# Kernel tuning notes

Hardware: AMD Instinct MI355X
Metric: run time of the kernel (lower is better)

Reference implementation:

```python
import jax, jax.numpy as jnp
from jax import lax
import numpy as np

ITER_ = 10
SMOOTH = 1.0

# ---------- soft skeletonization (clDice-style, 2D) ----------

def _max_pool(x, wh, ww):
    # x: [B,1,H,W]
    return lax.reduce_window(x, -jnp.inf, lax.max, (1, 1, wh, ww), (1, 1, 1, 1), 'SAME')

def _soft_erode(x):
    return jnp.minimum(-_max_pool(-x, 3, 1), -_max_pool(-x, 1, 3))

def _soft_dilate(x):
    return _max_pool(x, 3, 3)

def _soft_open(x):
    return _soft_dilate(_soft_erode(x))

def soft_skel(img, iters):
    skel = jax.nn.relu(img - _soft_open(img))
    for _ in range(iters):
        img = _soft_erode(img)
        delta = jax.nn.relu(img - _soft_open(img))
        skel = skel + jax.nn.relu(delta - skel * delta)
    return skel

# ---------- exact 2D Euclidean distance transform ----------

def _edt2d(mask):
    # mask: [H,W] bool, True = foreground. distance to nearest background pixel.
    H, W = mask.shape
    BIG = jnp.float32(H + W)
    z = ~mask  # background indicator
    def step(d, zr):
        d = jnp.where(zr, 0.0, jnp.minimum(d + 1.0, BIG))
        return d, d
    init = jnp.full((H,), BIG, jnp.float32)
    _, f = lax.scan(step, init, z.T)            # [W,H] forward along rows
    _, b = lax.scan(step, init, z.T[::-1])      # backward
    g = jnp.minimum(f, b[::-1]).T               # [H,W] 1D row distance
    ys = jnp.arange(H, dtype=jnp.float32)
    diff2 = (ys[:, None] - ys[None, :]) ** 2    # [H,H]
    # lower envelope over columns: d2[y,x] = min_y' g[y',x]^2 + (y-y')^2
    d2 = jnp.min(g[None, :, :] ** 2 + diff2[:, :, None], axis=1)  # [H,W]
    return jnp.sqrt(d2)

_edt_batched = jax.vmap(_edt2d)  # [B,H,W] bool -> [B,H,W] float

# ---------- cbDice pieces ----------

def combine_tensors(A, B, C):
    return jnp.where((A != 0) & (B == 0), A * C, B * C)

def get_weights(mask_input, skel_input, prob_flag):
    # mask_input/skel_input: [B,H,W] float
    mask = mask_input > 0.5
    skel = skel_input > 0.5
    dist = lax.stop_gradient(_edt_batched(mask))       # EDT of binary mask, non-diff
    distances = jnp.where(mask, dist, 0.0)
    skel_radius = jnp.where(skel, distances, 0.0)
    rmax = jnp.maximum(jnp.max(skel_radius, axis=(1, 2), keepdims=True), 1.0)
    rmin = jnp.maximum(jnp.min(skel_radius, axis=(1, 2), keepdims=True), 1.0)
    d_clip = jnp.minimum(distances, rmax)
    dist_map_norm = d_clip / rmax
    skel_R_norm = skel_radius / rmax
    I_norm = (rmax - skel_radius + rmin) / rmax        # dim == 2 branch
    I_norm = jnp.where(skel, I_norm, 0.0)
    if prob_flag:
        return dist_map_norm * mask_input, skel_R_norm * mask_input, I_norm * skel_input
    m = mask.astype(jnp.float32)
    s = skel.astype(jnp.float32)
    return dist_map_norm * m, skel_R_norm * m, I_norm * s

def soft_cb_dice_loss(y_pred, y_true):
    p = jax.nn.sigmoid(y_pred)                              # [B,1,H,W]
    pb = jnp.concatenate([1.0 - p, p], axis=1)              # [B,2,H,W]
    pp = jax.nn.softmax(pb, axis=1)[:, 1]                   # [B,H,W]
    yt = jnp.where(y_true > 0, 1.0, 0.0)[:, 0]              # [B,H,W]
    hard = lax.stop_gradient((pp > 0.5).astype(jnp.float32))
    skel_pred_hard = lax.stop_gradient(soft_skel(hard[:, None], ITER_)[:, 0])
    skel_true = lax.stop_gradient(soft_skel(yt[:, None], ITER_)[:, 0])
    skel_pred_prob = skel_pred_hard * pp
    q_vl, q_slvl, q_sl = get_weights(yt, skel_true, False)
    q_vp, q_spvp, q_sp = get_weights(pp, skel_pred_prob, True)
    w_tprec = (jnp.sum(q_sp * q_vl) + SMOOTH) / (jnp.sum(combine_tensors(q_spvp, q_slvl, q_sp)) + SMOOTH)
    w_tsens = (jnp.sum(q_sl * q_vp) + SMOOTH) / (jnp.sum(combine_tensors(q_slvl, q_spvp, q_sl)) + SMOOTH)
    return 1.0 - 2.0 * (w_tprec * w_tsens) / (w_tprec + w_tsens)

def setup_inputs() -> dict:
    key = jax.random.key(0)
    k1, k2 = jax.random.split(key)
    y_pred = jax.random.normal(k1, (4, 1, 256, 256), dtype=jnp.float32)
    y_true = jax.random.randint(k2, (4, 1, 256, 256), 0, 2, dtype=jnp.int32)
    return {"y_pred": y_pred, "y_true": y_true}

def reference(y_pred, y_true):
    return soft_cb_dice_loss(y_pred, y_true)
```

## Files before the change

kernel.cpp:

```cpp
#include <hip/hip_runtime.h>

typedef unsigned long long u64;

#define NIMG 4
#define H 256
#define W 256
#define NPIX (H*W)
#define NTOT (NIMG*NPIX)
#define WPR 4
#define WPI (H*WPR)
#define WPB (NIMG*WPI)
#define XT 16

__global__ void prep_kernel(const float* __restrict__ y_pred,
                            const int* __restrict__ y_true,
                            float* __restrict__ pp,
                            u64* __restrict__ mask_bits,
                            unsigned* __restrict__ rmm_u,
                            double* __restrict__ sums) {
  if (blockIdx.x == 0) {
    if (threadIdx.x < 16) rmm_u[threadIdx.x] = (threadIdx.x & 1) ? 0x7F800000u : 0u;
    else if (threadIdx.x < 20) sums[threadIdx.x - 16] = 0.0;
  }
  int i = blockIdx.x * 256 + threadIdx.x;
  float x = y_pred[i];
  float p = 1.0f / (1.0f + expf(-x));
  float q = 1.0f / (1.0f + expf(-(2.0f * p - 1.0f)));
  pp[i] = q;
  u64 bt = __ballot(y_true[i] > 0);
  u64 bp = __ballot(q > 0.5f);
  if ((threadIdx.x & 63) == 0) {
    mask_bits[i >> 6] = bt;
    mask_bits[WPB + (i >> 6)] = bp;
  }
}

__device__ __forceinline__ void erode_from(const u64 S[][WPR], int y, u64 out[WPR]) {
  u64 c[WPR], up[WPR], dn[WPR];
#pragma unroll
  for (int k = 0; k < WPR; ++k) {
    c[k]  = S[y][k];
    up[k] = (y > 0)     ? S[y-1][k] : ~0ULL;
    dn[k] = (y < H-1)   ? S[y+1][k] : ~0ULL;
  }
#pragma unroll
  for (int k = 0; k < WPR; ++k) {
    u64 l = (c[k] << 1) | ((k > 0)     ? (c[k-1] >> 63) : 1ULL);
    u64 r = (c[k] >> 1) | ((k < WPR-1) ? (c[k+1] << 63) : 0x8000000000000000ULL);
    out[k] = c[k] & up[k] & dn[k] & l & r;
  }
}

__device__ __forceinline__ void dilate_from(const u64 S[][WPR], int y, u64 out[WPR]) {
  u64 v[WPR];
#pragma unroll
  for (int k = 0; k < WPR; ++k) {
    u64 a = S[y][k];
    if (y > 0)   a |= S[y-1][k];
    if (y < H-1) a |= S[y+1][k];
    v[k] = a;
  }
#pragma unroll
  for (int k = 0; k < WPR; ++k) {
    u64 l = (v[k] << 1) | ((k > 0)     ? (v[k-1] >> 63) : 0ULL);
    u64 r = (v[k] >> 1) | ((k < WPR-1) ? (v[k+1] << 63) : 0ULL);
    out[k] = v[k] | l | r;
  }
}

__global__ void skel_kernel(const u64* __restrict__ mask_bits,
                            u64* __restrict__ skel_bits) {
  __shared__ u64 SA[H][WPR];
  __shared__ u64 SB[H][WPR];
  int y = threadIdx.x;
  int base = blockIdx.x * WPI;
  u64 a[WPR], cur[WPR], e[WPR], d[WPR], sk[WPR];
#pragma unroll
  for (int k = 0; k < WPR; ++k) { a[k] = mask_bits[base + y*WPR + k]; SA[y][k] = a[k]; }
  __syncthreads();
  erode_from(SA, y, e);
#pragma unroll
  for (int k = 0; k < WPR; ++k) SB[y][k] = e[k];
  __syncthreads();
  dilate_from(SB, y, d);
#pragma unroll
  for (int k = 0; k < WPR; ++k) { sk[k] = a[k] & ~d[k]; cur[k] = e[k]; }
  u64 (*P)[WPR] = SB;
  u64 (*Q)[WPR] = SA;
  for (int it = 0; it < 10; ++it) {
    erode_from(P, y, e);
#pragma unroll
    for (int k = 0; k < WPR; ++k) Q[y][k] = e[k];
    __syncthreads();
    dilate_from(Q, y, d);
#pragma unroll
    for (int k = 0; k < WPR; ++k) { sk[k] |= cur[k] & ~d[k]; cur[k] = e[k]; }
    u64 (*T)[WPR] = P; P = Q; Q = T;
  }
#pragma unroll
  for (int k = 0; k < WPR; ++k) skel_bits[base + y*WPR + k] = sk[k];
}

__global__ void edt_cols_kernel(const u64* __restrict__ mask_bits,
                                const u64* __restrict__ skel_bits,
                                float* __restrict__ edt,
                                unsigned* __restrict__ rmm_u) {
  __shared__ float col2[H][XT + 1];
  int bi = blockIdx.x >> 4;
  int xt = blockIdx.x & 15;
  int x0 = xt * XT;
  int kx = x0 >> 6;
  int sh0 = x0 & 63;
  int t = threadIdx.x;
  {
    int y = t;
    const u64* row = mask_bits + bi*WPI + y*WPR;
    u64 z[WPR];
#pragma unroll
    for (int k = 0; k < WPR; ++k) z[k] = ~row[k];
#pragma unroll
    for (int xx = 0; xx < XT; ++xx) {
      int x = x0 + xx;
      int bx = x & 63;
      int ld = 512;
      {
        u64 w = z[kx] & ((bx == 63) ? ~0ULL : ((1ULL << (bx+1)) - 1ULL));
        for (int k = kx; ; ) {
          if (w) { int pos = 63 - __builtin_clzll(w) + (k << 6); ld = x - pos; break; }
          if (--k < 0) break;
          w = z[k];
        }
      }
      int rd = 512;
      {
        u64 w = z[kx] & (~0ULL << bx);
        for (int k = kx; ; ) {
          if (w) { int pos = __builtin_ctzll(w) + (k << 6); rd = pos - x; break; }
          if (++k > WPR-1) break;
          w = z[k];
        }
      }
      int g = min(ld, rd);
      col2[y][xx] = (float)(g * g);
    }
  }
  __syncthreads();
  int x  = t & (XT - 1);
  int yg = t >> 4;
  float vmax = 0.0f, vmin = 3.0e38f;
#pragma unroll
  for (int j = 0; j < 16; ++j) {
    int y = yg * 16 + j;
    float best = col2[y][x];
    for (int k = 1; k < H; ++k) {
      float k2 = (float)(k * k);
      if (k2 >= best) break;
      int ym = y - k, yq = y + k;
      if (ym >= 0) best = fminf(best, col2[ym][x] + k2);
      if (yq < H)  best = fminf(best, col2[yq][x] + k2);
    }
    float dist = sqrtf(best);
    edt[bi*NPIX + y*W + x0 + x] = dist;
    u64 sw = skel_bits[bi*WPI + y*WPR + kx];
    int sb = (int)((sw >> (sh0 + x)) & 1ULL);
    float srad = sb ? dist : 0.0f;
    vmax = fmaxf(vmax, srad);
    vmin = fminf(vmin, srad);
  }
  for (int o = 32; o > 0; o >>= 1) {
    vmax = fmaxf(vmax, __shfl_down(vmax, o, 64));
    vmin = fminf(vmin, __shfl_down(vmin, o, 64));
  }
  __shared__ float smax[4], smin[4];
  int wave = t >> 6, lane = t & 63;
  if (lane == 0) { smax[wave] = vmax; smin[wave] = vmin; }
  __syncthreads();
  if (t == 0) {
    float mx = smax[0], mn = smin[0];
    for (int wv = 1; wv < 4; ++wv) { mx = fmaxf(mx, smax[wv]); mn = fminf(mn, smin[wv]); }
    atomicMax(&rmm_u[bi*2 + 0], __float_as_uint(mx));
    atomicMin(&rmm_u[bi*2 + 1], __float_as_uint(mn));
  }
}

__global__ void final_sum_kernel(const float* __restrict__ edt,
                                 const u64* __restrict__ mask_bits,
                                 const u64* __restrict__ skel_bits,
                                 const float* __restrict__ pp,
                                 const unsigned* __restrict__ rmm_u,
                                 double* __restrict__ sums) {
  int i0 = (blockIdx.x * 256 + threadIdx.x) * 4;
  int img = i0 >> 16;
  int wi = i0 >> 6;
  int b0 = i0 & 63;
  u64 mw_t = mask_bits[wi];
  u64 sw_t = skel_bits[wi];
  u64 sw_p = skel_bits[WPB + wi];
  float4 d_t4 = *(const float4*)(edt + i0);
  float4 d_p4 = *(const float4*)(edt + NTOT + i0);
  float4 pp4  = *(const float4*)(pp + i0);
  float rmax_t = fmaxf(__uint_as_float(rmm_u[img*2 + 0]), 1.0f);
  float rmin_t = fmaxf(__uint_as_float(rmm_u[img*2 + 1]), 1.0f);
  float rmax_p = fmaxf(__uint_as_float(rmm_u[(4+img)*2 + 0]), 1.0f);
  float rmin_p = fmaxf(__uint_as_float(rmm_u[(4+img)*2 + 1]), 1.0f);
  float t1 = 0.f, t2 = 0.f, t3 = 0.f, t4 = 0.f;
  float dts[4] = {d_t4.x, d_t4.y, d_t4.z, d_t4.w};
  float dps[4] = {d_p4.x, d_p4.y, d_p4.z, d_p4.w};
  float pps[4] = {pp4.x, pp4.y, pp4.z, pp4.w};
#pragma unroll
  for (int j = 0; j < 4; ++j) {
    int b = b0 + j;
    int m_t = (int)((mw_t >> b) & 1ULL);
    int s_t = (int)((sw_t >> b) & 1ULL);
    float distances_t = m_t ? dts[j] : 0.0f;
    float skelrad_t   = s_t ? distances_t : 0.0f;
    float dmn_t = fminf(distances_t, rmax_t) / rmax_t;
    float srn_t = skelrad_t / rmax_t;
    float In_t  = s_t ? (rmax_t - skelrad_t + rmin_t) / rmax_t : 0.0f;
    float q_vl   = m_t ? dmn_t : 0.0f;
    float q_slvl = m_t ? srn_t : 0.0f;
    float q_sl   = s_t ? In_t  : 0.0f;
    int s_pb = (int)((sw_p >> b) & 1ULL);
    float ppv = pps[j];
    float skel_in_p = s_pb ? ppv : 0.0f;
    bool msk_p = ppv > 0.5f;
    bool sk_p  = skel_in_p > 0.5f;
    float distances_p = msk_p ? dps[j] : 0.0f;
    float skelrad_p   = sk_p ? distances_p : 0.0f;
    float dmn_p = fminf(distances_p, rmax_p) / rmax_p;
    float srn_p = skelrad_p / rmax_p;
    float In_p  = sk_p ? (rmax_p - skelrad_p + rmin_p) / rmax_p : 0.0f;
    float q_vp   = dmn_p * ppv;
    float q_spvp = srn_p * ppv;
    float q_sp   = In_p * skel_in_p;
    t1 += q_sp * q_vl;
    t2 += (q_spvp != 0.0f && q_slvl == 0.0f) ? q_spvp * q_sp : q_slvl * q_sp;
    t3 += q_sl * q_vp;
    t4 += (q_slvl != 0.0f && q_spvp == 0.0f) ? q_slvl * q_sl : q_spvp * q_sl;
  }
  for (int o = 32; o > 0; o >>= 1) {
    t1 += __shfl_down(t1, o, 64);
    t2 += __shfl_down(t2, o, 64);
    t3 += __shfl_down(t3, o, 64);
    t4 += __shfl_down(t4, o, 64);
  }
  __shared__ float part[4][4];
  int wave = threadIdx.x >> 6, lane = threadIdx.x & 63;
  if (lane == 0) { part[wave][0]=t1; part[wave][1]=t2; part[wave][2]=t3; part[wave][3]=t4; }
  __syncthreads();
  if (threadIdx.x == 0) {
    float a0=0,a1=0,a2=0,a3=0;
    for (int wv = 0; wv < 4; ++wv) {
      a0 += part[wv][0]; a1 += part[wv][1]; a2 += part[wv][2]; a3 += part[wv][3];
    }
    atomicAdd(&sums[0], (double)a0);
    atomicAdd(&sums[1], (double)a1);
    atomicAdd(&sums[2], (double)a2);
    atomicAdd(&sums[3], (double)a3);
  }
}

__global__ void finalize_kernel(const double* __restrict__ sums,
                                float* __restrict__ out) {
  double wp  = (sums[0] + 1.0) / (sums[1] + 1.0);
  double wsn = (sums[2] + 1.0) / (sums[3] + 1.0);
  double loss = 1.0 - 2.0 * (wp * wsn) / (wp + wsn);
  out[0] = (float)loss;
}

extern "C" void kernel_launch(void* const* d_in, const int* in_sizes, int n_in,
                              void* d_out, int out_size, void* d_ws, size_t ws_size,
                              hipStream_t stream) {
  (void)in_sizes; (void)n_in; (void)out_size; (void)ws_size;
  const float* y_pred = (const float*)d_in[0];
  const int*   y_true = (const int*)d_in[1];
  float* out = (float*)d_out;
  char* ws = (char*)d_ws;

  float* pp        = (float*)(ws + 0);
  float* edt       = (float*)(ws + 1048576);
  u64*   mask_bits = (u64*)  (ws + 3145728);
  u64*   skel_bits = (u64*)  (ws + 3211264);
  unsigned* rmm_u  = (unsigned*)(ws + 3276800);
  double* sums     = (double*)(ws + 3276864);

  prep_kernel<<<NTOT/256, 256, 0, stream>>>(y_pred, y_true, pp, mask_bits, rmm_u, sums);
  skel_kernel<<<8, 256, 0, stream>>>(mask_bits, skel_bits);
  edt_cols_kernel<<<8*(W/XT), 256, 0, stream>>>(mask_bits, skel_bits, edt, rmm_u);
  final_sum_kernel<<<NTOT/1024, 256, 0, stream>>>(edt, mask_bits, skel_bits, pp, rmm_u, sums);
  finalize_kernel<<<1, 1, 0, stream>>>(sums, out);
}
```

Before: 95.78 us.

## Fuse all stages into one cooperative kernel with grid syncs

Result: slower. 143.9 us (+50.2%).

```diff
diff --git a/kernel.cpp b/kernel.cpp
--- a/kernel.cpp
+++ b/kernel.cpp
@@ -1,4 +1,7 @@
 #include <hip/hip_runtime.h>
+#include <hip/hip_cooperative_groups.h>
+
+namespace cg = cooperative_groups;
 
 typedef unsigned long long u64;
 
@@ -11,29 +14,9 @@
 #define WPI (H*WPR)
 #define WPB (NIMG*WPI)
 #define XT 16
-
-__global__ void prep_kernel(const float* __restrict__ y_pred,
-                            const int* __restrict__ y_true,
-                            float* __restrict__ pp,
-                            u64* __restrict__ mask_bits,
-                            unsigned* __restrict__ rmm_u,
-                            double* __restrict__ sums) {
-  if (blockIdx.x == 0) {
-    if (threadIdx.x < 16) rmm_u[threadIdx.x] = (threadIdx.x & 1) ? 0x7F800000u : 0u;
-    else if (threadIdx.x < 20) sums[threadIdx.x - 16] = 0.0;
-  }
-  int i = blockIdx.x * 256 + threadIdx.x;
-  float x = y_pred[i];
-  float p = 1.0f / (1.0f + expf(-x));
-  float q = 1.0f / (1.0f + expf(-(2.0f * p - 1.0f)));
-  pp[i] = q;
-  u64 bt = __ballot(y_true[i] > 0);
-  u64 bp = __ballot(q > 0.5f);
-  if ((threadIdx.x & 63) == 0) {
-    mask_bits[i >> 6] = bt;
-    mask_bits[WPB + (i >> 6)] = bp;
-  }
-}
+#define NEDT 128
+#define NSKEL 8
+#define NBLK (NEDT+NSKEL)
 
 __device__ __forceinline__ void erode_from(const u64 S[][WPR], int y, u64 out[WPR]) {
   u64 c[WPR], up[WPR], dn[WPR];
@@ -68,204 +51,248 @@
   }
 }
 
-__global__ void skel_kernel(const u64* __restrict__ mask_bits,
-                            u64* __restrict__ skel_bits) {
+__global__ void __launch_bounds__(256, 1) fused_kernel(
+    const float* __restrict__ y_pred, const int* __restrict__ y_true,
+    float* __restrict__ pp, u64* __restrict__ mask_bits, u64* __restrict__ skel_bits,
+    float* __restrict__ edt, unsigned* __restrict__ rmm_u, double* __restrict__ sums,
+    unsigned* __restrict__ done_cnt, float* __restrict__ out) {
+  cg::grid_group grid = cg::this_grid();
   __shared__ u64 SA[H][WPR];
   __shared__ u64 SB[H][WPR];
-  int y = threadIdx.x;
-  int base = blockIdx.x * WPI;
-  u64 a[WPR], cur[WPR], e[WPR], d[WPR], sk[WPR];
-#pragma unroll
-  for (int k = 0; k < WPR; ++k) { a[k] = mask_bits[base + y*WPR + k]; SA[y][k] = a[k]; }
-  __syncthreads();
-  erode_from(SA, y, e);
-#pragma unroll
-  for (int k = 0; k < WPR; ++k) SB[y][k] = e[k];
-  __syncthreads();
-  dilate_from(SB, y, d);
-#pragma unroll
-  for (int k = 0; k < WPR; ++k) { sk[k] = a[k] & ~d[k]; cur[k] = e[k]; }
-  u64 (*P)[WPR] = SB;
-  u64 (*Q)[WPR] = SA;
-  for (int it = 0; it < 10; ++it) {
-    erode_from(P, y, e);
-#pragma unroll
-    for (int k = 0; k < WPR; ++k) Q[y][k] = e[k];
-    __syncthreads();
-    dilate_from(Q, y, d);
-#pragma unroll
-    for (int k = 0; k < WPR; ++k) { sk[k] |= cur[k] & ~d[k]; cur[k] = e[k]; }
-    u64 (*T)[WPR] = P; P = Q; Q = T;
-  }
-#pragma unroll
-  for (int k = 0; k < WPR; ++k) skel_bits[base + y*WPR + k] = sk[k];
-}
-
-__global__ void edt_cols_kernel(const u64* __restrict__ mask_bits,
-                                const u64* __restrict__ skel_bits,
-                                float* __restrict__ edt,
-                                unsigned* __restrict__ rmm_u) {
   __shared__ float col2[H][XT + 1];
-  int bi = blockIdx.x >> 4;
-  int xt = blockIdx.x & 15;
-  int x0 = xt * XT;
-  int kx = x0 >> 6;
-  int sh0 = x0 & 63;
+  __shared__ float redf[4][4];
   int t = threadIdx.x;
-  {
+
+  if (blockIdx.x < NEDT) {
+    if (blockIdx.x == 0) {
+      if (t < 16) rmm_u[t] = (t & 1) ? 0x7F800000u : 0u;
+      else if (t < 20) sums[t - 16] = 0.0;
+      else if (t == 20) *done_cnt = 0u;
+    }
+    int g = blockIdx.x * 256 + t;
+#pragma unroll
+    for (int j = 0; j < 8; ++j) {
+      int i = (j << 15) + g;
+      float x = y_pred[i];
+      float p = 1.0f / (1.0f + expf(-x));
+      float q = 1.0f / (1.0f + expf(-(2.0f * p - 1.0f)));
+      pp[i] = q;
+      u64 bt = __ballot(y_true[i] > 0);
+      u64 bp = __ballot(q > 0.5f);
+      if ((t & 63) == 0) {
+        mask_bits[i >> 6] = bt;
+        mask_bits[WPB + (i >> 6)] = bp;
+      }
+    }
+  }
+  grid.sync();
+
+  float dist_r[16];
+  if (blockIdx.x >= NEDT) {
     int y = t;
-    const u64* row = mask_bits + bi*WPI + y*WPR;
-    u64 z[WPR];
-#pragma unroll
-    for (int k = 0; k < WPR; ++k) z[k] = ~row[k];
-#pragma unroll
-    for (int xx = 0; xx < XT; ++xx) {
-      int x = x0 + xx;
-      int bx = x & 63;
-      int ld = 512;
-      {
-        u64 w = z[kx] & ((bx == 63) ? ~0ULL : ((1ULL << (bx+1)) - 1ULL));
-        for (int k = kx; ; ) {
-          if (w) { int pos = 63 - __builtin_clzll(w) + (k << 6); ld = x - pos; break; }
-          if (--k < 0) break;
-          w = z[k];
+    int base = (blockIdx.x - NEDT) * WPI;
+    u64 a[WPR], cur[WPR], e[WPR], d[WPR], sk[WPR];
+#pragma unroll
+    for (int k = 0; k < WPR; ++k) { a[k] = mask_bits[base + y*WPR + k]; SA[y][k] = a[k]; }
+    __syncthreads();
+    erode_from(SA, y, e);
+#pragma unroll
+    for (int k = 0; k < WPR; ++k) SB[y][k] = e[k];
+    __syncthreads();
+    dilate_from(SB, y, d);
+#pragma unroll
+    for (int k = 0; k < WPR; ++k) { sk[k] = a[k] & ~d[k]; cur[k] = e[k]; }
+    u64 (*P)[WPR] = SB;
+    u64 (*Q)[WPR] = SA;
+    for (int it = 0; it < 10; ++it) {
+      erode_from(P, y, e);
+#pragma unroll
+      for (int k = 0; k < WPR; ++k) Q[y][k] = e[k];
+      __syncthreads();
+      dilate_from(Q, y, d);
+#pragma unroll
+      for (int k = 0; k < WPR; ++k) { sk[k] |= cur[k] & ~d[k]; cur[k] = e[k]; }
+      u64 (*T)[WPR] = P; P = Q; Q = T;
+    }
+#pragma unroll
+    for (int k = 0; k < WPR; ++k) skel_bits[base + y*WPR + k] = sk[k];
+  } else {
+    int bi = blockIdx.x >> 4;
+    int xt = blockIdx.x & 15;
+    int x0 = xt * XT;
+    int kx = x0 >> 6;
+    {
+      int y = t;
+      const u64* row = mask_bits + bi*WPI + y*WPR;
+      u64 z[WPR];
+#pragma unroll
+      for (int k = 0; k < WPR; ++k) z[k] = ~row[k];
+#pragma unroll
+      for (int xx = 0; xx < XT; ++xx) {
+        int x = x0 + xx;
+        int bx = x & 63;
+        int ld = 512;
+        {
+          u64 w = z[kx] & ((bx == 63) ? ~0ULL : ((1ULL << (bx+1)) - 1ULL));
+          for (int k = kx; ; ) {
+            if (w) { int pos = 63 - __builtin_clzll(w) + (k << 6); ld = x - pos; break; }
+            if (--k < 0) break;
+            w = z[k];
+          }
         }
-      }
-      int rd = 512;
-      {
-        u64 w = z[kx] & (~0ULL << bx);
-        for (int k = kx; ; ) {
-          if (w) { int pos = __builtin_ctzll(w) + (k << 6); rd = pos - x; break; }
-          if (++k > WPR-1) break;
-          w = z[k];
+        int rd = 512;
+        {
+          u64 w = z[kx] & (~0ULL << bx);
+          for (int k = kx; ; ) {
+            if (w) { int pos = __builtin_ctzll(w) + (k << 6); rd = pos - x; break; }
+            if (++k > WPR-1) break;
+            w = z[k];
+          }
         }
-      }
-      int g = min(ld, rd);
-      col2[y][xx] = (float)(g * g);
-    }
-  }
-  __syncthreads();
-  int x  = t & (XT - 1);
-  int yg = t >> 4;
-  float vmax = 0.0f, vmin = 3.0e38f;
-#pragma unroll
-  for (int j = 0; j < 16; ++j) {
-    int y = yg * 16 + j;
-    float best = col2[y][x];
-    for (int k = 1; k < H; ++k) {
-      float k2 = (float)(k * k);
-      if (k2 >= best) break;
-      int ym = y - k, yq = y + k;
-      if (ym >= 0) best = fminf(best, col2[ym][x] + k2);
-      if (yq < H)  best = fminf(best, col2[yq][x] + k2);
-    }
-    float dist = sqrtf(best);
-    edt[bi*NPIX + y*W + x0 + x] = dist;
-    u64 sw = skel_bits[bi*WPI + y*WPR + kx];
-    int sb = (int)((sw >> (sh0 + x)) & 1ULL);
-    float srad = sb ? dist : 0.0f;
-    vmax = fmaxf(vmax, srad);
-    vmin = fminf(vmin, srad);
-  }
-  for (int o = 32; o > 0; o >>= 1) {
-    vmax = fmaxf(vmax, __shfl_down(vmax, o, 64));
-    vmin = fminf(vmin, __shfl_down(vmin, o, 64));
-  }
-  __shared__ float smax[4], smin[4];
-  int wave = t >> 6, lane = t & 63;
-  if (lane == 0) { smax[wave] = vmax; smin[wave] = vmin; }
-  __syncthreads();
-  if (t == 0) {
-    float mx = smax[0], mn = smin[0];
-    for (int wv = 1; wv < 4; ++wv) { mx = fmaxf(mx, smax[wv]); mn = fminf(mn, smin[wv]); }
-    atomicMax(&rmm_u[bi*2 + 0], __float_as_uint(mx));
-    atomicMin(&rmm_u[bi*2 + 1], __float_as_uint(mn));
-  }
-}
-
-__global__ void final_sum_kernel(const float* __restrict__ edt,
-                                 const u64* __restrict__ mask_bits,
-                                 const u64* __restrict__ skel_bits,
-                                 const float* __restrict__ pp,
-                                 const unsigned* __restrict__ rmm_u,
-                                 double* __restrict__ sums) {
-  int i0 = (blockIdx.x * 256 + threadIdx.x) * 4;
-  int img = i0 >> 16;
-  int wi = i0 >> 6;
-  int b0 = i0 & 63;
-  u64 mw_t = mask_bits[wi];
-  u64 sw_t = skel_bits[wi];
-  u64 sw_p = skel_bits[WPB + wi];
-  float4 d_t4 = *(const float4*)(edt + i0);
-  float4 d_p4 = *(const float4*)(edt + NTOT + i0);
-  float4 pp4  = *(const float4*)(pp + i0);
-  float rmax_t = fmaxf(__uint_as_float(rmm_u[img*2 + 0]), 1.0f);
-  float rmin_t = fmaxf(__uint_as_float(rmm_u[img*2 + 1]), 1.0f);
-  float rmax_p = fmaxf(__uint_as_float(rmm_u[(4+img)*2 + 0]), 1.0f);
-  float rmin_p = fmaxf(__uint_as_float(rmm_u[(4+img)*2 + 1]), 1.0f);
-  float t1 = 0.f, t2 = 0.f, t3 = 0.f, t4 = 0.f;
-  float dts[4] = {d_t4.x, d_t4.y, d_t4.z, d_t4.w};
-  float dps[4] = {d_p4.x, d_p4.y, d_p4.z, d_p4.w};
-  float pps[4] = {pp4.x, pp4.y, pp4.z, pp4.w};
-#pragma unroll
-  for (int j = 0; j < 4; ++j) {
-    int b = b0 + j;
-    int m_t = (int)((mw_t >> b) & 1ULL);
-    int s_t = (int)((sw_t >> b) & 1ULL);
-    float distances_t = m_t ? dts[j] : 0.0f;
-    float skelrad_t   = s_t ? distances_t : 0.0f;
-    float dmn_t = fminf(distances_t, rmax_t) / rmax_t;
-    float srn_t = skelrad_t / rmax_t;
-    float In_t  = s_t ? (rmax_t - skelrad_t + rmin_t) / rmax_t : 0.0f;
-    float q_vl   = m_t ? dmn_t : 0.0f;
-    float q_slvl = m_t ? srn_t : 0.0f;
-    float q_sl   = s_t ? In_t  : 0.0f;
-    int s_pb = (int)((sw_p >> b) & 1ULL);
-    float ppv = pps[j];
-    float skel_in_p = s_pb ? ppv : 0.0f;
-    bool msk_p = ppv > 0.5f;
-    bool sk_p  = skel_in_p > 0.5f;
-    float distances_p = msk_p ? dps[j] : 0.0f;
-    float skelrad_p   = sk_p ? distances_p : 0.0f;
-    float dmn_p = fminf(distances_p, rmax_p) / rmax_p;
-    float srn_p = skelrad_p / rmax_p;
-    float In_p  = sk_p ? (rmax_p - skelrad_p + rmin_p) / rmax_p : 0.0f;
-    float q_vp   = dmn_p * ppv;
-    float q_spvp = srn_p * ppv;
-    float q_sp   = In_p * skel_in_p;
-    t1 += q_sp * q_vl;
-    t2 += (q_spvp != 0.0f && q_slvl == 0.0f) ? q_spvp * q_sp : q_slvl * q_sp;
-    t3 += q_sl * q_vp;
-    t4 += (q_slvl != 0.0f && q_spvp == 0.0f) ? q_slvl * q_sl : q_spvp * q_sl;
-  }
-  for (int o = 32; o > 0; o >>= 1) {
-    t1 += __shfl_down(t1, o, 64);
-    t2 += __shfl_down(t2, o, 64);
-    t3 += __shfl_down(t3, o, 64);
-    t4 += __shfl_down(t4, o, 64);
-  }
-  __shared__ float part[4][4];
-  int wave = threadIdx.x >> 6, lane = threadIdx.x & 63;
-  if (lane == 0) { part[wave][0]=t1; part[wave][1]=t2; part[wave][2]=t3; part[wave][3]=t4; }
-  __syncthreads();
-  if (threadIdx.x == 0) {
-    float a0=0,a1=0,a2=0,a3=0;
-    for (int wv = 0; wv < 4; ++wv) {
-      a0 += part[wv][0]; a1 += part[wv][1]; a2 += part[wv][2]; a3 += part[wv][3];
-    }
-    atomicAdd(&sums[0], (double)a0);
-    atomicAdd(&sums[1], (double)a1);
-    atomicAdd(&sums[2], (double)a2);
-    atomicAdd(&sums[3], (double)a3);
-  }
-}
-
-__global__ void finalize_kernel(const double* __restrict__ sums,
-                                float* __restrict__ out) {
-  double wp  = (sums[0] + 1.0) / (sums[1] + 1.0);
-  double wsn = (sums[2] + 1.0) / (sums[3] + 1.0);
-  double loss = 1.0 - 2.0 * (wp * wsn) / (wp + wsn);
-  out[0] = (float)loss;
+        int g = min(ld, rd);
+        col2[y][xx] = (float)(g * g);
+      }
+    }
+    __syncthreads();
+    int x  = t & (XT - 1);
+    int yg = t >> 4;
+#pragma unroll
+    for (int j = 0; j < 16; ++j) {
+      int y = yg * 16 + j;
+      float best = col2[y][x];
+      for (int k = 1; k < H; ++k) {
+        float k2 = (float)(k * k);
+        if (k2 >= best) break;
+        int ym = y - k, yq = y + k;
+        if (ym >= 0) best = fminf(best, col2[ym][x] + k2);
+        if (yq < H)  best = fminf(best, col2[yq][x] + k2);
+      }
+      float dist = sqrtf(best);
+      dist_r[j] = dist;
+      edt[bi*NPIX + y*W + x0 + x] = dist;
+    }
+  }
+  grid.sync();
+
+  if (blockIdx.x < NEDT) {
+    int bi = blockIdx.x >> 4;
+    int xt = blockIdx.x & 15;
+    int x0 = xt * XT;
+    int kx = x0 >> 6;
+    int sh0 = x0 & 63;
+    int x  = t & (XT - 1);
+    int yg = t >> 4;
+    float vmax = 0.0f, vmin = 3.0e38f;
+#pragma unroll
+    for (int j = 0; j < 16; ++j) {
+      int y = yg * 16 + j;
+      u64 sw = skel_bits[bi*WPI + y*WPR + kx];
+      int sb = (int)((sw >> (sh0 + x)) & 1ULL);
+      float srad = sb ? dist_r[j] : 0.0f;
+      vmax = fmaxf(vmax, srad);
+      vmin = fminf(vmin, srad);
+    }
+    for (int o = 32; o > 0; o >>= 1) {
+      vmax = fmaxf(vmax, __shfl_down(vmax, o, 64));
+      vmin = fminf(vmin, __shfl_down(vmin, o, 64));
+    }
+    int wave = t >> 6, lane = t & 63;
+    if (lane == 0) { redf[wave][0] = vmax; redf[wave][1] = vmin; }
+    __syncthreads();
+    if (t == 0) {
+      float mx = redf[0][0], mn = redf[0][1];
+      for (int wv = 1; wv < 4; ++wv) { mx = fmaxf(mx, redf[wv][0]); mn = fminf(mn, redf[wv][1]); }
+      atomicMax(&rmm_u[bi*2 + 0], __float_as_uint(mx));
+      atomicMin(&rmm_u[bi*2 + 1], __float_as_uint(mn));
+    }
+  }
+  grid.sync();
+
+  if (blockIdx.x < NEDT) {
+    int g = blockIdx.x * 256 + t;
+    int i0 = g * 8;
+    int img = i0 >> 16;
+    int wi  = i0 >> 6;
+    int b0  = i0 & 63;
+    u64 mw_t = mask_bits[wi];
+    u64 sw_t = skel_bits[wi];
+    u64 sw_p = skel_bits[WPB + wi];
+    float4 dt0 = *(const float4*)(edt + i0);
+    float4 dt1 = *(const float4*)(edt + i0 + 4);
+    float4 dp0 = *(const float4*)(edt + NTOT + i0);
+    float4 dp1 = *(const float4*)(edt + NTOT + i0 + 4);
+    float4 pq0 = *(const float4*)(pp + i0);
+    float4 pq1 = *(const float4*)(pp + i0 + 4);
+    float rmax_t = fmaxf(__uint_as_float(rmm_u[img*2 + 0]), 1.0f);
+    float rmin_t = fmaxf(__uint_as_float(rmm_u[img*2 + 1]), 1.0f);
+    float rmax_p = fmaxf(__uint_as_float(rmm_u[(4+img)*2 + 0]), 1.0f);
+    float rmin_p = fmaxf(__uint_as_float(rmm_u[(4+img)*2 + 1]), 1.0f);
+    float dts[8] = {dt0.x,dt0.y,dt0.z,dt0.w,dt1.x,dt1.y,dt1.z,dt1.w};
+    float dps[8] = {dp0.x,dp0.y,dp0.z,dp0.w,dp1.x,dp1.y,dp1.z,dp1.w};
+    float pps[8] = {pq0.x,pq0.y,pq0.z,pq0.w,pq1.x,pq1.y,pq1.z,pq1.w};
+    float q1 = 0.f, q2 = 0.f, q3 = 0.f, q4 = 0.f;
+#pragma unroll
+    for (int j = 0; j < 8; ++j) {
+      int b = b0 + j;
+      int m_t = (int)((mw_t >> b) & 1ULL);
+      int s_t = (int)((sw_t >> b) & 1ULL);
+      float distances_t = m_t ? dts[j] : 0.0f;
+      float skelrad_t   = s_t ? distances_t : 0.0f;
+      float dmn_t = fminf(distances_t, rmax_t) / rmax_t;
+      float srn_t = skelrad_t / rmax_t;
+      float In_t  = s_t ? (rmax_t - skelrad_t + rmin_t) / rmax_t : 0.0f;
+      float q_vl   = m_t ? dmn_t : 0.0f;
+      float q_slvl = m_t ? srn_t : 0.0f;
+      float q_sl   = s_t ? In_t  : 0.0f;
+      int s_pb = (int)((sw_p >> b) & 1ULL);
+      float ppv = pps[j];
+      float skel_in_p = s_pb ? ppv : 0.0f;
+      bool msk_p = ppv > 0.5f;
+      bool sk_p  = skel_in_p > 0.5f;
+      float distances_p = msk_p ? dps[j] : 0.0f;
+      float skelrad_p   = sk_p ? distances_p : 0.0f;
+      float dmn_p = fminf(distances_p, rmax_p) / rmax_p;
+      float srn_p = skelrad_p / rmax_p;
+      float In_p  = sk_p ? (rmax_p - skelrad_p + rmin_p) / rmax_p : 0.0f;
+      float q_vp   = dmn_p * ppv;
+      float q_spvp = srn_p * ppv;
+      float q_sp   = In_p * skel_in_p;
+      q1 += q_sp * q_vl;
+      q2 += (q_spvp != 0.0f && q_slvl == 0.0f) ? q_spvp * q_sp : q_slvl * q_sp;
+      q3 += q_sl * q_vp;
+      q4 += (q_slvl != 0.0f && q_spvp == 0.0f) ? q_slvl * q_sl : q_spvp * q_sl;
+    }
+    for (int o = 32; o > 0; o >>= 1) {
+      q1 += __shfl_down(q1, o, 64);
+      q2 += __shfl_down(q2, o, 64);
+      q3 += __shfl_down(q3, o, 64);
+      q4 += __shfl_down(q4, o, 64);
+    }
+    int wave = t >> 6, lane = t & 63;
+    if (lane == 0) { redf[wave][0]=q1; redf[wave][1]=q2; redf[wave][2]=q3; redf[wave][3]=q4; }
+    __syncthreads();
+    if (t == 0) {
+      float a0=0,a1=0,a2=0,a3=0;
+      for (int wv = 0; wv < 4; ++wv) {
+        a0 += redf[wv][0]; a1 += redf[wv][1]; a2 += redf[wv][2]; a3 += redf[wv][3];
+      }
+      atomicAdd(&sums[0], (double)a0);
+      atomicAdd(&sums[1], (double)a1);
+      atomicAdd(&sums[2], (double)a2);
+      atomicAdd(&sums[3], (double)a3);
+      __threadfence();
+      unsigned c = atomicAdd(done_cnt, 1u);
+      if (c == NEDT - 1) {
+        double s0 = atomicAdd(&sums[0], 0.0);
+        double s1 = atomicAdd(&sums[1], 0.0);
+        double s2 = atomicAdd(&sums[2], 0.0);
+        double s3 = atomicAdd(&sums[3], 0.0);
+        double wp  = (s0 + 1.0) / (s1 + 1.0);
+        double wsn = (s2 + 1.0) / (s3 + 1.0);
+        out[0] = (float)(1.0 - 2.0 * (wp * wsn) / (wp + wsn));
+      }
+    }
+  }
 }
 
 extern "C" void kernel_launch(void* const* d_in, const int* in_sizes, int n_in,
@@ -283,10 +310,11 @@
   u64*   skel_bits = (u64*)  (ws + 3211264);
   unsigned* rmm_u  = (unsigned*)(ws + 3276800);
   double* sums     = (double*)(ws + 3276864);
-
-  prep_kernel<<<NTOT/256, 256, 0, stream>>>(y_pred, y_true, pp, mask_bits, rmm_u, sums);
-  skel_kernel<<<8, 256, 0, stream>>>(mask_bits, skel_bits);
-  edt_cols_kernel<<<8*(W/XT), 256, 0, stream>>>(mask_bits, skel_bits, edt, rmm_u);
-  final_sum_kernel<<<NTOT/1024, 256, 0, stream>>>(edt, mask_bits, skel_bits, pp, rmm_u, sums);
-  finalize_kernel<<<1, 1, 0, stream>>>(sums, out);
+  unsigned* done_cnt = (unsigned*)(ws + 3276896);
+
+  void* args[] = { (void*)&y_pred, (void*)&y_true, (void*)&pp, (void*)&mask_bits,
+                   (void*)&skel_bits, (void*)&edt, (void*)&rmm_u, (void*)&sums,
+                   (void*)&done_cnt, (void*)&out };
+  hipLaunchCooperativeKernel((void*)fused_kernel, dim3(NBLK), dim3(256),
+                             args, 0, stream);
 }
```

## Fuse skeleton and EDT kernels with inter-block flags; fold finalize into last block

Applied to the files above, without the earlier changes.

After: 102.7 us. 1.07x slower.

```diff
diff --git a/kernel.cpp b/kernel.cpp
--- a/kernel.cpp
+++ b/kernel.cpp
@@ -11,16 +11,51 @@
 #define WPI (H*WPR)
 #define WPB (NIMG*WPI)
 #define XT 16
-
-__global__ void prep_kernel(const float* __restrict__ y_pred,
-                            const int* __restrict__ y_true,
-                            float* __restrict__ pp,
-                            u64* __restrict__ mask_bits,
-                            unsigned* __restrict__ rmm_u,
-                            double* __restrict__ sums) {
+#define NSKEL 8
+#define NEDT 128
+#define NB2 (NSKEL+NEDT)
+#define NB3 (NTOT/1024)
+
+__device__ __forceinline__ void erode_from(const u64 S[][WPR], int y, u64 out[WPR]) {
+  u64 c[WPR], up[WPR], dn[WPR];
+#pragma unroll
+  for (int k = 0; k < WPR; ++k) {
+    c[k]  = S[y][k];
+    up[k] = (y > 0)     ? S[y-1][k] : ~0ULL;
+    dn[k] = (y < H-1)   ? S[y+1][k] : ~0ULL;
+  }
+#pragma unroll
+  for (int k = 0; k < WPR; ++k) {
+    u64 l = (c[k] << 1) | ((k > 0)     ? (c[k-1] >> 63) : 1ULL);
+    u64 r = (c[k] >> 1) | ((k < WPR-1) ? (c[k+1] << 63) : 0x8000000000000000ULL);
+    out[k] = c[k] & up[k] & dn[k] & l & r;
+  }
+}
+
+__device__ __forceinline__ void dilate_from(const u64 S[][WPR], int y, u64 out[WPR]) {
+  u64 v[WPR];
+#pragma unroll
+  for (int k = 0; k < WPR; ++k) {
+    u64 a = S[y][k];
+    if (y > 0)   a |= S[y-1][k];
+    if (y < H-1) a |= S[y+1][k];
+    v[k] = a;
+  }
+#pragma unroll
+  for (int k = 0; k < WPR; ++k) {
+    u64 l = (v[k] << 1) | ((k > 0)     ? (v[k-1] >> 63) : 0ULL);
+    u64 r = (v[k] >> 1) | ((k < WPR-1) ? (v[k+1] << 63) : 0ULL);
+    out[k] = v[k] | l | r;
+  }
+}
+
+__global__ void __launch_bounds__(256) prep_kernel(
+    const float* __restrict__ y_pred, const int* __restrict__ y_true,
+    float* __restrict__ pp, u64* __restrict__ mask_bits,
+    double* __restrict__ sums, unsigned* __restrict__ cnts) {
   if (blockIdx.x == 0) {
-    if (threadIdx.x < 16) rmm_u[threadIdx.x] = (threadIdx.x & 1) ? 0x7F800000u : 0u;
-    else if (threadIdx.x < 20) sums[threadIdx.x - 16] = 0.0;
+    if (threadIdx.x < 4) sums[threadIdx.x] = 0.0;
+    else if (threadIdx.x < 13) cnts[threadIdx.x - 4] = 0u;
   }
   int i = blockIdx.x * 256 + threadIdx.x;
   float x = y_pred[i];
@@ -35,160 +70,152 @@
   }
 }
 
-__device__ __forceinline__ void erode_from(const u64 S[][WPR], int y, u64 out[WPR]) {
-  u64 c[WPR], up[WPR], dn[WPR];
-#pragma unroll
-  for (int k = 0; k < WPR; ++k) {
-    c[k]  = S[y][k];
-    up[k] = (y > 0)     ? S[y-1][k] : ~0ULL;
-    dn[k] = (y < H-1)   ? S[y+1][k] : ~0ULL;
-  }
-#pragma unroll
-  for (int k = 0; k < WPR; ++k) {
-    u64 l = (c[k] << 1) | ((k > 0)     ? (c[k-1] >> 63) : 1ULL);
-    u64 r = (c[k] >> 1) | ((k < WPR-1) ? (c[k+1] << 63) : 0x8000000000000000ULL);
-    out[k] = c[k] & up[k] & dn[k] & l & r;
-  }
-}
-
-__device__ __forceinline__ void dilate_from(const u64 S[][WPR], int y, u64 out[WPR]) {
-  u64 v[WPR];
-#pragma unroll
-  for (int k = 0; k < WPR; ++k) {
-    u64 a = S[y][k];
-    if (y > 0)   a |= S[y-1][k];
-    if (y < H-1) a |= S[y+1][k];
-    v[k] = a;
-  }
-#pragma unroll
-  for (int k = 0; k < WPR; ++k) {
-    u64 l = (v[k] << 1) | ((k > 0)     ? (v[k-1] >> 63) : 0ULL);
-    u64 r = (v[k] >> 1) | ((k < WPR-1) ? (v[k+1] << 63) : 0ULL);
-    out[k] = v[k] | l | r;
-  }
-}
-
-__global__ void skel_kernel(const u64* __restrict__ mask_bits,
-                            u64* __restrict__ skel_bits) {
+__global__ void __launch_bounds__(256, 1) morpho_kernel(
+    const u64* __restrict__ mask_bits, u64* __restrict__ skel_bits,
+    float* __restrict__ edt, float* __restrict__ rmm_f,
+    unsigned* __restrict__ cnts) {
   __shared__ u64 SA[H][WPR];
   __shared__ u64 SB[H][WPR];
-  int y = threadIdx.x;
-  int base = blockIdx.x * WPI;
-  u64 a[WPR], cur[WPR], e[WPR], d[WPR], sk[WPR];
-#pragma unroll
-  for (int k = 0; k < WPR; ++k) { a[k] = mask_bits[base + y*WPR + k]; SA[y][k] = a[k]; }
-  __syncthreads();
-  erode_from(SA, y, e);
-#pragma unroll
-  for (int k = 0; k < WPR; ++k) SB[y][k] = e[k];
-  __syncthreads();
-  dilate_from(SB, y, d);
-#pragma unroll
-  for (int k = 0; k < WPR; ++k) { sk[k] = a[k] & ~d[k]; cur[k] = e[k]; }
-  u64 (*P)[WPR] = SB;
-  u64 (*Q)[WPR] = SA;
-  for (int it = 0; it < 10; ++it) {
-    erode_from(P, y, e);
-#pragma unroll
-    for (int k = 0; k < WPR; ++k) Q[y][k] = e[k];
-    __syncthreads();
-    dilate_from(Q, y, d);
-#pragma unroll
-    for (int k = 0; k < WPR; ++k) { sk[k] |= cur[k] & ~d[k]; cur[k] = e[k]; }
-    u64 (*T)[WPR] = P; P = Q; Q = T;
-  }
-#pragma unroll
-  for (int k = 0; k < WPR; ++k) skel_bits[base + y*WPR + k] = sk[k];
-}
-
-__global__ void edt_cols_kernel(const u64* __restrict__ mask_bits,
-                                const u64* __restrict__ skel_bits,
-                                float* __restrict__ edt,
-                                unsigned* __restrict__ rmm_u) {
   __shared__ float col2[H][XT + 1];
-  int bi = blockIdx.x >> 4;
-  int xt = blockIdx.x & 15;
-  int x0 = xt * XT;
-  int kx = x0 >> 6;
-  int sh0 = x0 & 63;
+  __shared__ float smax[4], smin[4];
   int t = threadIdx.x;
-  {
+
+  if (blockIdx.x < NSKEL) {
+    int bi = blockIdx.x;
     int y = t;
-    const u64* row = mask_bits + bi*WPI + y*WPR;
-    u64 z[WPR];
-#pragma unroll
-    for (int k = 0; k < WPR; ++k) z[k] = ~row[k];
-#pragma unroll
-    for (int xx = 0; xx < XT; ++xx) {
-      int x = x0 + xx;
-      int bx = x & 63;
-      int ld = 512;
-      {
-        u64 w = z[kx] & ((bx == 63) ? ~0ULL : ((1ULL << (bx+1)) - 1ULL));
-        for (int k = kx; ; ) {
-          if (w) { int pos = 63 - __builtin_clzll(w) + (k << 6); ld = x - pos; break; }
-          if (--k < 0) break;
-          w = z[k];
+    int base = bi * WPI;
+    u64 a[WPR], cur[WPR], e[WPR], d[WPR], sk[WPR];
+#pragma unroll
+    for (int k = 0; k < WPR; ++k) { a[k] = mask_bits[base + y*WPR + k]; SA[y][k] = a[k]; }
+    __syncthreads();
+    erode_from(SA, y, e);
+#pragma unroll
+    for (int k = 0; k < WPR; ++k) SB[y][k] = e[k];
+    __syncthreads();
+    dilate_from(SB, y, d);
+#pragma unroll
+    for (int k = 0; k < WPR; ++k) { sk[k] = a[k] & ~d[k]; cur[k] = e[k]; }
+    u64 (*P)[WPR] = SB;
+    u64 (*Q)[WPR] = SA;
+    for (int it = 0; it < 10; ++it) {
+      erode_from(P, y, e);
+#pragma unroll
+      for (int k = 0; k < WPR; ++k) Q[y][k] = e[k];
+      __syncthreads();
+      dilate_from(Q, y, d);
+#pragma unroll
+      for (int k = 0; k < WPR; ++k) { sk[k] |= cur[k] & ~d[k]; cur[k] = e[k]; }
+      u64 (*T)[WPR] = P; P = Q; Q = T;
+    }
+#pragma unroll
+    for (int k = 0; k < WPR; ++k) skel_bits[base + y*WPR + k] = sk[k];
+    __syncthreads();
+#pragma unroll
+    for (int k = 0; k < WPR; ++k) SA[y][k] = sk[k];
+    if (t == 0) {
+      while (__hip_atomic_load(&cnts[bi], __ATOMIC_ACQUIRE,
+                               __HIP_MEMORY_SCOPE_AGENT) < 16u)
+        __builtin_amdgcn_s_sleep(8);
+    }
+    __syncthreads();
+    __threadfence();
+    const float* epx = edt + bi * NPIX;
+    float vmax = 0.0f, vmin = 3.0e38f;
+    for (int it2 = 0; it2 < 64; ++it2) {
+      int p0 = it2 * 1024 + t * 4;
+      float4 d4 = *(const float4*)(epx + p0);
+      int row = p0 >> 8;
+      u64 w = SA[row][(p0 & 255) >> 6];
+      int sh = p0 & 63;
+      float ds[4] = {d4.x, d4.y, d4.z, d4.w};
+#pragma unroll
+      for (int j = 0; j < 4; ++j) {
+        int bit = (int)((w >> (sh + j)) & 1ULL);
+        float srad = bit ? ds[j] : 0.0f;
+        vmax = fmaxf(vmax, srad);
+        vmin = fminf(vmin, srad);
+      }
+    }
+    for (int o = 32; o > 0; o >>= 1) {
+      vmax = fmaxf(vmax, __shfl_down(vmax, o, 64));
+      vmin = fminf(vmin, __shfl_down(vmin, o, 64));
+    }
+    int wave = t >> 6, lane = t & 63;
+    if (lane == 0) { smax[wave] = vmax; smin[wave] = vmin; }
+    __syncthreads();
+    if (t == 0) {
+      float mx = smax[0], mn = smin[0];
+      for (int wv = 1; wv < 4; ++wv) { mx = fmaxf(mx, smax[wv]); mn = fminf(mn, smin[wv]); }
+      rmm_f[bi*2 + 0] = mx;
+      rmm_f[bi*2 + 1] = mn;
+    }
+  } else {
+    int bt = blockIdx.x - NSKEL;
+    int bi = bt >> 4;
+    int xt = bt & 15;
+    int x0 = xt * XT;
+    int kx = x0 >> 6;
+    {
+      int y = t;
+      const u64* row = mask_bits + bi*WPI + y*WPR;
+      u64 z[WPR];
+#pragma unroll
+      for (int k = 0; k < WPR; ++k) z[k] = ~row[k];
+#pragma unroll
+      for (int xx = 0; xx < XT; ++xx) {
+        int x = x0 + xx;
+        int bx = x & 63;
+        int ld = 512;
+        {
+          u64 w = z[kx] & ((bx == 63) ? ~0ULL : ((1ULL << (bx+1)) - 1ULL));
+          for (int k = kx; ; ) {
+            if (w) { int pos = 63 - __builtin_clzll(w) + (k << 6); ld = x - pos; break; }
+            if (--k < 0) break;
+            w = z[k];
+          }
         }
+        int rd = 512;
+        {
+          u64 w = z[kx] & (~0ULL << bx);
+          for (int k = kx; ; ) {
+            if (w) { int pos = __builtin_ctzll(w) + (k << 6); rd = pos - x; break; }
+            if (++k > WPR-1) break;
+            w = z[k];
+          }
+        }
+        int g = min(ld, rd);
+        col2[y][xx] = (float)(g * g);
       }
-      int rd = 512;
-      {
-        u64 w = z[kx] & (~0ULL << bx);
-        for (int k = kx; ; ) {
-          if (w) { int pos = __builtin_ctzll(w) + (k << 6); rd = pos - x; break; }
-          if (++k > WPR-1) break;
-          w = z[k];
-        }
+    }
+    __syncthreads();
+    int x  = t & (XT - 1);
+    int yg = t >> 4;
+#pragma unroll
+    for (int j = 0; j < 16; ++j) {
+      int y = yg * 16 + j;
+      float best = col2[y][x];
+      for (int k = 1; k < H; ++k) {
+        float k2 = (float)(k * k);
+        if (k2 >= best) break;
+        int ym = y - k, yq = y + k;
+        if (ym >= 0) best = fminf(best, col2[ym][x] + k2);
+        if (yq < H)  best = fminf(best, col2[yq][x] + k2);
       }
-      int g = min(ld, rd);
-      col2[y][xx] = (float)(g * g);
-    }
-  }
-  __syncthreads();
-  int x  = t & (XT - 1);
-  int yg = t >> 4;
-  float vmax = 0.0f, vmin = 3.0e38f;
-#pragma unroll
-  for (int j = 0; j < 16; ++j) {
-    int y = yg * 16 + j;
-    float best = col2[y][x];
-    for (int k = 1; k < H; ++k) {
-      float k2 = (float)(k * k);
-      if (k2 >= best) break;
-      int ym = y - k, yq = y + k;
-      if (ym >= 0) best = fminf(best, col2[ym][x] + k2);
-      if (yq < H)  best = fminf(best, col2[yq][x] + k2);
-    }
-    float dist = sqrtf(best);
-    edt[bi*NPIX + y*W + x0 + x] = dist;
-    u64 sw = skel_bits[bi*WPI + y*WPR + kx];
-    int sb = (int)((sw >> (sh0 + x)) & 1ULL);
-    float srad = sb ? dist : 0.0f;
-    vmax = fmaxf(vmax, srad);
-    vmin = fminf(vmin, srad);
-  }
-  for (int o = 32; o > 0; o >>= 1) {
-    vmax = fmaxf(vmax, __shfl_down(vmax, o, 64));
-    vmin = fminf(vmin, __shfl_down(vmin, o, 64));
-  }
-  __shared__ float smax[4], smin[4];
-  int wave = t >> 6, lane = t & 63;
-  if (lane == 0) { smax[wave] = vmax; smin[wave] = vmin; }
-  __syncthreads();
-  if (t == 0) {
-    float mx = smax[0], mn = smin[0];
-    for (int wv = 1; wv < 4; ++wv) { mx = fmaxf(mx, smax[wv]); mn = fminf(mn, smin[wv]); }
-    atomicMax(&rmm_u[bi*2 + 0], __float_as_uint(mx));
-    atomicMin(&rmm_u[bi*2 + 1], __float_as_uint(mn));
-  }
-}
-
-__global__ void final_sum_kernel(const float* __restrict__ edt,
-                                 const u64* __restrict__ mask_bits,
-                                 const u64* __restrict__ skel_bits,
-                                 const float* __restrict__ pp,
-                                 const unsigned* __restrict__ rmm_u,
-                                 double* __restrict__ sums) {
+      edt[bi*NPIX + y*W + x0 + x] = sqrtf(best);
+    }
+    __syncthreads();
+    if (t == 0) {
+      __threadfence();
+      atomicAdd(&cnts[bi], 1u);
+    }
+  }
+}
+
+__global__ void __launch_bounds__(256) final_kernel(
+    const float* __restrict__ edt, const u64* __restrict__ mask_bits,
+    const u64* __restrict__ skel_bits, const float* __restrict__ pp,
+    const float* __restrict__ rmm_f, double* __restrict__ sums,
+    unsigned* __restrict__ cnts, float* __restrict__ out) {
   int i0 = (blockIdx.x * 256 + threadIdx.x) * 4;
   int img = i0 >> 16;
   int wi = i0 >> 6;
@@ -199,10 +226,10 @@
   float4 d_t4 = *(const float4*)(edt + i0);
   float4 d_p4 = *(const float4*)(edt + NTOT + i0);
   float4 pp4  = *(const float4*)(pp + i0);
-  float rmax_t = fmaxf(__uint_as_float(rmm_u[img*2 + 0]), 1.0f);
-  float rmin_t = fmaxf(__uint_as_float(rmm_u[img*2 + 1]), 1.0f);
-  float rmax_p = fmaxf(__uint_as_float(rmm_u[(4+img)*2 + 0]), 1.0f);
-  float rmin_p = fmaxf(__uint_as_float(rmm_u[(4+img)*2 + 1]), 1.0f);
+  float rmax_t = fmaxf(rmm_f[img*2 + 0], 1.0f);
+  float rmin_t = fmaxf(rmm_f[img*2 + 1], 1.0f);
+  float rmax_p = fmaxf(rmm_f[(4+img)*2 + 0], 1.0f);
+  float rmin_p = fmaxf(rmm_f[(4+img)*2 + 1], 1.0f);
   float t1 = 0.f, t2 = 0.f, t3 = 0.f, t4 = 0.f;
   float dts[4] = {d_t4.x, d_t4.y, d_t4.z, d_t4.w};
   float dps[4] = {d_p4.x, d_p4.y, d_p4.z, d_p4.w};
@@ -257,15 +284,18 @@
     atomicAdd(&sums[1], (double)a1);
     atomicAdd(&sums[2], (double)a2);
     atomicAdd(&sums[3], (double)a3);
-  }
-}
-
-__global__ void finalize_kernel(const double* __restrict__ sums,
-                                float* __restrict__ out) {
-  double wp  = (sums[0] + 1.0) / (sums[1] + 1.0);
-  double wsn = (sums[2] + 1.0) / (sums[3] + 1.0);
-  double loss = 1.0 - 2.0 * (wp * wsn) / (wp + wsn);
-  out[0] = (float)loss;
+    __threadfence();
+    unsigned c = atomicAdd(&cnts[8], 1u);
+    if (c == NB3 - 1) {
+      double s0 = atomicAdd(&sums[0], 0.0);
+      double s1 = atomicAdd(&sums[1], 0.0);
+      double s2 = atomicAdd(&sums[2], 0.0);
+      double s3 = atomicAdd(&sums[3], 0.0);
+      double wp  = (s0 + 1.0) / (s1 + 1.0);
+      double wsn = (s2 + 1.0) / (s3 + 1.0);
+      out[0] = (float)(1.0 - 2.0 * (wp * wsn) / (wp + wsn));
+    }
+  }
 }
 
 extern "C" void kernel_launch(void* const* d_in, const int* in_sizes, int n_in,
@@ -281,12 +311,11 @@
   float* edt       = (float*)(ws + 1048576);
   u64*   mask_bits = (u64*)  (ws + 3145728);
   u64*   skel_bits = (u64*)  (ws + 3211264);
-  unsigned* rmm_u  = (unsigned*)(ws + 3276800);
+  float* rmm_f     = (float*)(ws + 3276800);
   double* sums     = (double*)(ws + 3276864);
-
-  prep_kernel<<<NTOT/256, 256, 0, stream>>>(y_pred, y_true, pp, mask_bits, rmm_u, sums);
-  skel_kernel<<<8, 256, 0, stream>>>(mask_bits, skel_bits);
-  edt_cols_kernel<<<8*(W/XT), 256, 0, stream>>>(mask_bits, skel_bits, edt, rmm_u);
-  final_sum_kernel<<<NTOT/1024, 256, 0, stream>>>(edt, mask_bits, skel_bits, pp, rmm_u, sums);
-  finalize_kernel<<<1, 1, 0, stream>>>(sums, out);
-}
+  unsigned* cnts   = (unsigned*)(ws + 3276896);
+
+  prep_kernel<<<NTOT/256, 256, 0, stream>>>(y_pred, y_true, pp, mask_bits, sums, cnts);
+  morpho_kernel<<<NB2, 256, 0, stream>>>(mask_bits, skel_bits, edt, rmm_f, cnts);
+  final_kernel<<<NB3, 256, 0, stream>>>(edt, mask_bits, skel_bits, pp, rmm_f, sums, cnts, out);
+}
```
